# Kernel tuning notes

Hardware: AMD Instinct MI355X
Metric: run time of the kernel (lower is better)

Reference implementation:

```python
import jax, jax.numpy as jnp
import numpy as np

C = 32       # dim_features
D1 = 1024    # line grid resolution (dim1)
D2 = 256     # lowres plane resolution (dim2)
M = 64       # hidden width m
H = 1024
W = 1024
RESX = 1024.0
RESY = 1024.0


def setup_inputs() -> dict:
    key = jax.random.key(0)
    ks = jax.random.split(key, 8)
    coords = jax.random.uniform(ks[0], (H, W, 2), dtype=jnp.float32) * RESX
    # operation == 'multiply' init: rand*0.15 + 0.1
    line_feature_x = jax.random.uniform(ks[1], (C, D1), dtype=jnp.float32) * 0.15 + 0.1
    line_feature_y = jax.random.uniform(ks[2], (C, D1), dtype=jnp.float32) * 0.15 + 0.1
    plane_feature = jax.random.normal(ks[3], (C, D2, D2), dtype=jnp.float32) * 0.01
    W1 = jax.random.normal(ks[4], (M, C), dtype=jnp.float32) * (1.0 / np.sqrt(C))
    b1 = jnp.zeros((M,), dtype=jnp.float32)
    W2 = jax.random.normal(ks[5], (1, M), dtype=jnp.float32) * (1.0 / np.sqrt(M))
    b2 = jnp.zeros((1,), dtype=jnp.float32)
    return {"coords": coords, "line_feature_x": line_feature_x,
            "line_feature_y": line_feature_y, "plane_feature": plane_feature,
            "W1": W1, "b1": b1, "W2": W2, "b2": b2}


def _interp_line(table, gnorm):
    # table: [C, L]; gnorm: [H, W] in [-1, 1].
    # grid_sample(mode=bilinear, padding_mode=border, align_corners=True) on a
    # [1, C, L, 1] input reduces to 1D linear interp along L with clamped coords.
    L = table.shape[1]
    pos = jnp.clip((gnorm + 1.0) * 0.5 * (L - 1), 0.0, float(L - 1))
    i0 = jnp.minimum(jnp.floor(pos).astype(jnp.int32), L - 2)
    w = pos - i0.astype(pos.dtype)           # [H, W]
    return table[:, i0] * (1.0 - w) + table[:, i0 + 1] * w  # [C, H, W]


def _interp_plane(plane, xn, yn):
    # plane: [C, D, D]; xn/yn: [H, W] in [-1, 1].
    # grid_sample(mode=bilinear, padding_mode=zeros, align_corners=True).
    D = plane.shape[-1]
    px = (xn + 1.0) * 0.5 * (D - 1)
    py = (yn + 1.0) * 0.5 * (D - 1)
    x0 = jnp.floor(px).astype(jnp.int32)
    y0 = jnp.floor(py).astype(jnp.int32)
    wx = px - x0.astype(px.dtype)
    wy = py - y0.astype(py.dtype)

    def gather(yi, xi):
        valid = (xi >= 0) & (xi < D) & (yi >= 0) & (yi < D)   # zeros padding
        xc = jnp.clip(xi, 0, D - 1)
        yc = jnp.clip(yi, 0, D - 1)
        return plane[:, yc, xc] * valid                       # [C, H, W]

    return (gather(y0, x0) * (1.0 - wy) * (1.0 - wx)
            + gather(y0, x0 + 1) * (1.0 - wy) * wx
            + gather(y0 + 1, x0) * wy * (1.0 - wx)
            + gather(y0 + 1, x0 + 1) * wy * wx)


def reference(coords, line_feature_x, line_feature_y, plane_feature, W1, b1, W2, b2):
    xn = coords[..., 0] * 2.0 / RESX - 1.0   # [H, W]
    yn = coords[..., 1] * 2.0 / RESY - 1.0
    fx = _interp_line(line_feature_x, xn)    # [C, H, W]
    fy = _interp_line(line_feature_y, yn)    # [C, H, W]
    fp = _interp_plane(plane_feature, xn, yn)  # [C, H, W]
    # operation == 'multiply', mode == 'lowres'
    feat = (fx * fy + fp).transpose(1, 2, 0)  # [H, W, C]
    # nonconvex decoder: Linear(C->M) + ReLU + Linear(M->1)
    h = jax.nn.relu(jnp.einsum('hwc,mc->hwm', feat, W1) + b1)
    out = jnp.einsum('hwm,om->hwo', h, W2) + b2
    return out[..., 0]                        # [H, W]
```

## Files before the change

kernel.cpp:

```cpp
#include <hip/hip_runtime.h>

#define NC   32
#define ND1  1024
#define ND2  256
#define NM   64
#define NPIX (1024 * 1024)
#define NBUCK 256
#define CAP  4608
#define NSLOT (NBUCK * CAP)
#define PW   18
#define PPAD 33
#define FBLK 3
#define FTH  512

__device__ __forceinline__ int clampi(int v, int lo, int hi) {
    return min(max(v, lo), hi);
}

__global__ __launch_bounds__(256) void pass1_prepare(
    const float* __restrict__ plane, const float* __restrict__ lfx,
    const float* __restrict__ lfy, float* __restrict__ pl_t,
    float* __restrict__ lx_t, float* __restrict__ ly_t, int* __restrict__ cursor)
{
    __shared__ float tile[32][65];
    const int blk = blockIdx.x, tid = threadIdx.x;
    const float* in; float* out; int N, pos0;
    if (blk < 1024)      { in = plane; out = pl_t; N = 65536; pos0 = blk * 64; }
    else if (blk < 1040) { in = lfx;   out = lx_t; N = 1024;  pos0 = (blk - 1024) * 64; }
    else if (blk < 1056) { in = lfy;   out = ly_t; N = 1024;  pos0 = (blk - 1040) * 64; }
    else { if (tid < NBUCK) cursor[tid] = tid * CAP; return; }
#pragma unroll
    for (int r = 0; r < 8; ++r) {
        int c = r * 4 + (tid >> 6), p = tid & 63;
        tile[c][p] = in[c * N + pos0 + p];
    }
    __syncthreads();
#pragma unroll
    for (int r = 0; r < 8; ++r) {
        int p = r * 8 + (tid >> 5), c = tid & 31;
        out[(pos0 + p) * 32 + c] = tile[c][p];
    }
}

__global__ __launch_bounds__(1024) void scatter_slack(
    const float2* __restrict__ coords, int* __restrict__ cursor,
    float4* __restrict__ slots)
{
    __shared__ int h[NBUCK];
    __shared__ int basew[NBUCK];
    const int t = threadIdx.x;
    if (t < NBUCK) h[t] = 0;
    __syncthreads();
    const int base_i = blockIdx.x * 4096;
    float2 xy[4]; int cell[4];
#pragma unroll
    for (int r = 0; r < 4; ++r) {
        xy[r] = coords[base_i + r * 1024 + t];
        const int xi = clampi((int)xy[r].x, 0, 1023);
        const int yi = clampi((int)xy[r].y, 0, 1023);
        cell[r] = ((yi >> 6) << 4) | (xi >> 6);
        atomicAdd(&h[cell[r]], 1);
    }
    __syncthreads();
    if (t < NBUCK) {
        const int n = h[t];
        basew[t] = n ? atomicAdd(&cursor[t], n) : 0;
    }
    __syncthreads();
    if (t < NBUCK) h[t] = 0;
    __syncthreads();
#pragma unroll
    for (int r = 0; r < 4; ++r) {
        const int c   = cell[r];
        const int off = atomicAdd(&h[c], 1);
        const int dst = min(basew[c] + off, NSLOT - 1);
        slots[dst] = make_float4(xy[r].x, xy[r].y,
                                 __int_as_float(base_i + r * 1024 + t), 0.0f);
    }
}

__global__ __launch_bounds__(FTH) void fused_bucket(
    const float4* __restrict__ slots, const int* __restrict__ cursor,
    const float* __restrict__ lx,
    const float* __restrict__ ly,
    const float* __restrict__ pl,
    const float* __restrict__ W1, const float* __restrict__ b1,
    const float* __restrict__ W2, const float* __restrict__ b2,
    float* __restrict__ out)
{
    const int b    = blockIdx.x / FBLK;
    const int part = blockIdx.x - b * FBLK;
    const int t    = threadIdx.x;
    const int bx = b & 15, by = b >> 4;
    const int px0 = (int)(bx * 15.9375f);
    const int py0 = (int)(by * 15.9375f);

    __shared__ float pls[PW * PW * PPAD];
    for (int i = t; i < PW * PW * 8; i += FTH) {
        const int tex = i >> 3, k = i & 7;
        const int ty = tex / PW, tx = tex - ty * PW;
        const int gy = min(py0 + ty, ND2 - 1), gx = min(px0 + tx, ND2 - 1);
        const float4 v = ((const float4*)pl)[((gy << 8) + gx) * 8 + k];
        float* d = &pls[tex * PPAD + k * 4];
        d[0] = v.x; d[1] = v.y; d[2] = v.z; d[3] = v.w;
    }
    __syncthreads();

    const int base  = b * CAP;
    const int count = min(cursor[b] - base, CAP);
    const int s_end = (part + 1) * (CAP / FBLK);
    for (int s = part * (CAP / FBLK) + t; s < s_end; s += FTH) {
        if (s >= count) break;
        const float4 rec = slots[base + s];
        const float x = rec.x, y = rec.y;
        const int pix = __float_as_int(rec.z);

        const float xn = x * (2.0f / 1024.0f) - 1.0f;
        const float yn = y * (2.0f / 1024.0f) - 1.0f;

        float posx = fminf(fmaxf((xn + 1.0f) * 0.5f * 1023.0f, 0.0f), 1023.0f);
        int   ix   = min((int)posx, 1022);
        float wx   = posx - (float)ix;
        float omwx = 1.0f - wx;
        float posy = fminf(fmaxf((yn + 1.0f) * 0.5f * 1023.0f, 0.0f), 1023.0f);
        int   iy   = min((int)posy, 1022);
        float wy   = posy - (float)iy;
        float omwy = 1.0f - wy;

        float px  = (xn + 1.0f) * 0.5f * 255.0f;
        float py  = (yn + 1.0f) * 0.5f * 255.0f;
        float fx0 = floorf(px), fy0 = floorf(py);
        int   x0 = (int)fx0, y0 = (int)fy0;
        float pwx = px - fx0, pwy = py - fy0;
        int   x1 = x0 + 1, y1 = y0 + 1;
        float vx0 = (x0 >= 0 && x0 < ND2) ? 1.0f : 0.0f;
        float vx1 = (x1 >= 0 && x1 < ND2) ? 1.0f : 0.0f;
        float vy0 = (y0 >= 0 && y0 < ND2) ? 1.0f : 0.0f;
        float vy1 = (y1 >= 0 && y1 < ND2) ? 1.0f : 0.0f;
        int xc0 = clampi(x0, 0, ND2 - 1), xc1 = clampi(x1, 0, ND2 - 1);
        int yc0 = clampi(y0, 0, ND2 - 1), yc1 = clampi(y1, 0, ND2 - 1);
        float w00 = (1.0f - pwy) * (1.0f - pwx) * vy0 * vx0;
        float w01 = (1.0f - pwy) * pwx          * vy0 * vx1;
        float w10 = pwy          * (1.0f - pwx) * vy1 * vx0;
        float w11 = pwy          * pwx          * vy1 * vx1;

        const int tx0i = xc0 - px0, tx1i = xc1 - px0;
        const int ty0i = yc0 - py0, ty1i = yc1 - py0;
        const float* t00 = &pls[(ty0i * PW + tx0i) * PPAD];
        const float* t01 = &pls[(ty0i * PW + tx1i) * PPAD];
        const float* t10 = &pls[(ty1i * PW + tx0i) * PPAD];
        const float* t11 = &pls[(ty1i * PW + tx1i) * PPAD];

        const float4* ax0 = (const float4*)(lx + ix * NC);
        const float4* ax1 = (const float4*)(lx + (ix + 1) * NC);
        const float4* ay0 = (const float4*)(ly + iy * NC);
        const float4* ay1 = (const float4*)(ly + (iy + 1) * NC);

        float feat[NC];
#pragma unroll
        for (int k = 0; k < 8; ++k) {
            const float4 a0 = ax0[k], a1 = ax1[k];
            const float4 c0 = ay0[k], c1 = ay1[k];
            const int cb = k * 4;
#define FC(j, comp)                                                          \
            {                                                                \
                float fxv = a0.comp * omwx + a1.comp * wx;                   \
                float fyv = c0.comp * omwy + c1.comp * wy;                   \
                float fpv = t00[cb + j] * w00 + t01[cb + j] * w01 +          \
                            t10[cb + j] * w10 + t11[cb + j] * w11;           \
                feat[cb + j] = fxv * fyv + fpv;                              \
            }
            FC(0, x) FC(1, y) FC(2, z) FC(3, w)
#undef FC
        }

        float acc = b2[0];
#pragma unroll 4
        for (int m = 0; m < NM; ++m) {
            const float4* wrow = (const float4*)(W1 + m * NC);
            float a = b1[m];
#pragma unroll
            for (int k = 0; k < 8; ++k) {
                const float4 wv = wrow[k];
                a = fmaf(feat[k * 4 + 0], wv.x, a);
                a = fmaf(feat[k * 4 + 1], wv.y, a);
                a = fmaf(feat[k * 4 + 2], wv.z, a);
                a = fmaf(feat[k * 4 + 3], wv.w, a);
            }
            acc = fmaf(fmaxf(a, 0.0f), W2[m], acc);
        }
        out[pix] = acc;
    }
}

template <int MODE>
__global__ __launch_bounds__(256) void fused_forward(
    const float* __restrict__ coords, const float* __restrict__ lx,
    const float* __restrict__ ly, const float* __restrict__ pl,
    const float* __restrict__ W1, const float* __restrict__ b1,
    const float* __restrict__ W2, const float* __restrict__ b2,
    float* __restrict__ out)
{
    const int i = blockIdx.x * 256 + threadIdx.x;
    const float2 xy = reinterpret_cast<const float2*>(coords)[i];
    const float xn = xy.x * (2.0f / 1024.0f) - 1.0f;
    const float yn = xy.y * (2.0f / 1024.0f) - 1.0f;

    float posx = fminf(fmaxf((xn + 1.0f) * 0.5f * 1023.0f, 0.0f), 1023.0f);
    int   ix   = min((int)posx, 1022);
    float wx   = posx - (float)ix, omwx = 1.0f - wx;
    float posy = fminf(fmaxf((yn + 1.0f) * 0.5f * 1023.0f, 0.0f), 1023.0f);
    int   iy   = min((int)posy, 1022);
    float wy   = posy - (float)iy, omwy = 1.0f - wy;

    float px  = (xn + 1.0f) * 0.5f * 255.0f;
    float py  = (yn + 1.0f) * 0.5f * 255.0f;
    float fx0 = floorf(px), fy0 = floorf(py);
    int   x0 = (int)fx0, y0 = (int)fy0;
    float pwx = px - fx0, pwy = py - fy0;
    int   x1 = x0 + 1, y1 = y0 + 1;
    float vx0 = (x0 >= 0 && x0 < ND2) ? 1.0f : 0.0f;
    float vx1 = (x1 >= 0 && x1 < ND2) ? 1.0f : 0.0f;
    float vy0 = (y0 >= 0 && y0 < ND2) ? 1.0f : 0.0f;
    float vy1 = (y1 >= 0 && y1 < ND2) ? 1.0f : 0.0f;
    int xc0 = clampi(x0, 0, ND2 - 1), xc1 = clampi(x1, 0, ND2 - 1);
    int yc0 = clampi(y0, 0, ND2 - 1), yc1 = clampi(y1, 0, ND2 - 1);
    float w00 = (1.0f - pwy) * (1.0f - pwx) * vy0 * vx0;
    float w01 = (1.0f - pwy) * pwx          * vy0 * vx1;
    float w10 = pwy          * (1.0f - pwx) * vy1 * vx0;
    float w11 = pwy          * pwx          * vy1 * vx1;

    float feat[NC];
    if (MODE == 1) {
        const float4* ax0 = (const float4*)(lx + ix * NC);
        const float4* ax1 = (const float4*)(lx + (ix + 1) * NC);
        const float4* ay0 = (const float4*)(ly + iy * NC);
        const float4* ay1 = (const float4*)(ly + (iy + 1) * NC);
        const float4* p00 = (const float4*)(pl + (yc0 * ND2 + xc0) * NC);
        const float4* p01 = (const float4*)(pl + (yc0 * ND2 + xc1) * NC);
        const float4* p10 = (const float4*)(pl + (yc1 * ND2 + xc0) * NC);
        const float4* p11 = (const float4*)(pl + (yc1 * ND2 + xc1) * NC);
#pragma unroll
        for (int k = 0; k < 8; ++k) {
            float4 a0 = ax0[k], a1 = ax1[k], c0 = ay0[k], c1 = ay1[k];
            float4 q00 = p00[k], q01 = p01[k], q10 = p10[k], q11 = p11[k];
#define FC(j, comp)                                                          \
            {                                                                \
                float fxv = a0.comp * omwx + a1.comp * wx;                   \
                float fyv = c0.comp * omwy + c1.comp * wy;                   \
                float fpv = q00.comp * w00 + q01.comp * w01 +                \
                            q10.comp * w10 + q11.comp * w11;                 \
                feat[k * 4 + j] = fxv * fyv + fpv;                           \
            }
            FC(0, x) FC(1, y) FC(2, z) FC(3, w)
#undef FC
        }
    } else {
#pragma unroll
        for (int c = 0; c < NC; ++c) {
            float a0 = lx[c * ND1 + ix], a1 = lx[c * ND1 + ix + 1];
            float c0 = ly[c * ND1 + iy], c1 = ly[c * ND1 + iy + 1];
            const float* ps = pl + c * (ND2 * ND2);
            float q00 = ps[yc0 * ND2 + xc0], q01 = ps[yc0 * ND2 + xc1];
            float q10 = ps[yc1 * ND2 + xc0], q11 = ps[yc1 * ND2 + xc1];
            feat[c] = (a0 * omwx + a1 * wx) * (c0 * omwy + c1 * wy)
                    + (q00 * w00 + q01 * w01 + q10 * w10 + q11 * w11);
        }
    }

    float acc = b2[0];
#pragma unroll 4
    for (int m = 0; m < NM; ++m) {
        const float4* wrow = (const float4*)(W1 + m * NC);
        float a = b1[m];
#pragma unroll
        for (int k = 0; k < 8; ++k) {
            float4 wv = wrow[k];
            a = fmaf(feat[k * 4 + 0], wv.x, a);
            a = fmaf(feat[k * 4 + 1], wv.y, a);
            a = fmaf(feat[k * 4 + 2], wv.z, a);
            a = fmaf(feat[k * 4 + 3], wv.w, a);
        }
        acc = fmaf(fmaxf(a, 0.0f), W2[m], acc);
    }
    out[i] = acc;
}

extern "C" void kernel_launch(void* const* d_in, const int* in_sizes, int n_in,
                              void* d_out, int out_size, void* d_ws, size_t ws_size,
                              hipStream_t stream) {
    const float* coords = (const float*)d_in[0];
    const float* lfx    = (const float*)d_in[1];
    const float* lfy    = (const float*)d_in[2];
    const float* plane  = (const float*)d_in[3];
    const float* W1     = (const float*)d_in[4];
    const float* b1     = (const float*)d_in[5];
    const float* W2     = (const float*)d_in[6];
    const float* b2     = (const float*)d_in[7];
    float* out = (float*)d_out;

    const size_t planeBytes = (size_t)ND2 * ND2 * NC * sizeof(float);
    const size_t lineBytes  = (size_t)ND1 * NC * sizeof(float);
    const size_t slotsBytes = (size_t)NSLOT * sizeof(float4);
    const size_t needTrans  = planeBytes + 2 * lineBytes;
    const size_t needFull   = needTrans + slotsBytes + NBUCK * sizeof(int);

    if (ws_size >= needFull) {
        char* p = (char*)d_ws;
        float*  pl_t   = (float*)p;   p += planeBytes;
        float*  lx_t   = (float*)p;   p += lineBytes;
        float*  ly_t   = (float*)p;   p += lineBytes;
        float4* slots  = (float4*)p;  p += slotsBytes;
        int*    cursor = (int*)p;

        pass1_prepare<<<1057, 256, 0, stream>>>(plane, lfx, lfy,
                                                pl_t, lx_t, ly_t, cursor);
        scatter_slack<<<NPIX / 4096, 1024, 0, stream>>>((const float2*)coords,
                                                        cursor, slots);
        fused_bucket<<<NBUCK * FBLK, FTH, 0, stream>>>(slots, cursor, lx_t, ly_t,
                                                       pl_t, W1, b1, W2, b2, out);
    } else if (ws_size >= needTrans) {
        float* pl_t = (float*)d_ws;
        float* lx_t = (float*)((char*)d_ws + planeBytes);
        float* ly_t = lx_t + ND1 * NC;
        pass1_prepare<<<1056, 256, 0, stream>>>(plane, lfx, lfy,
                                                pl_t, lx_t, ly_t, nullptr);
        fused_forward<1><<<NPIX / 256, 256, 0, stream>>>(
            coords, lx_t, ly_t, pl_t, W1, b1, W2, b2, out);
    } else {
        fused_forward<0><<<NPIX / 256, 256, 0, stream>>>(
            coords, lfx, lfy, plane, W1, b1, W2, b2, out);
    }
}
```

Measured before the change: 187.0 us.

## Compute decoder MLP with split-bf16 MFMA and load plane tile directly

Replaces the per-thread scalar 32x64 MLP in the bucketed kernel with wave-level MFMA 16x16x32 bf16 ops. Each wave handles 16 pixels, lanes split the channel dimension, and a hi/lo bf16 split (three MFMAs) approximates fp32 accuracy. The second layer is reduced with lane shuffles. The plane tile is now read straight from the original channel-major plane into shared memory, so the full plane transpose in the prepare pass is skipped and that pass shrinks to the line tables plus the cursor init. In exchange there is extra pack/shuffle work and slightly reduced precision, and the plane loads into shared memory become strided.

```diff
diff --git a/kernel.cpp b/kernel.cpp
--- a/kernel.cpp
+++ b/kernel.cpp
@@ -9,12 +9,32 @@
 #define CAP  4608
 #define NSLOT (NBUCK * CAP)
 #define PW   18
-#define PPAD 33
+#define PPADF 36
 #define FBLK 3
 #define FTH  512
+#define PART_SLOTS (CAP / FBLK)
+#define PART_CHUNKS (PART_SLOTS/16)
+
+typedef __attribute__((ext_vector_type(8))) short bf16x8;
+typedef __attribute__((ext_vector_type(4))) float f32x4;
 
 __device__ __forceinline__ int clampi(int v, int lo, int hi) {
     return min(max(v, lo), hi);
+}
+
+__device__ __forceinline__ void pack_hilo(const float* f, bf16x8& hi, bf16x8& lo) {
+    union { unsigned int u[4]; bf16x8 v; } H, L;
+#pragma unroll
+    for (int j = 0; j < 4; ++j) {
+        unsigned int b0 = __float_as_uint(f[2 * j]);
+        unsigned int b1 = __float_as_uint(f[2 * j + 1]);
+        unsigned int h0 = b0 & 0xFFFF0000u, h1 = b1 & 0xFFFF0000u;
+        H.u[j] = (h0 >> 16) | h1;
+        float l0 = f[2 * j]     - __uint_as_float(h0);
+        float l1 = f[2 * j + 1] - __uint_as_float(h1);
+        L.u[j] = (__float_as_uint(l0) >> 16) | (__float_as_uint(l1) & 0xFFFF0000u);
+    }
+    hi = H.v; lo = L.v;
 }
 
 __global__ __launch_bounds__(256) void pass1_prepare(
@@ -25,10 +45,10 @@
     __shared__ float tile[32][65];
     const int blk = blockIdx.x, tid = threadIdx.x;
     const float* in; float* out; int N, pos0;
-    if (blk < 1024)      { in = plane; out = pl_t; N = 65536; pos0 = blk * 64; }
-    else if (blk < 1040) { in = lfx;   out = lx_t; N = 1024;  pos0 = (blk - 1024) * 64; }
-    else if (blk < 1056) { in = lfy;   out = ly_t; N = 1024;  pos0 = (blk - 1040) * 64; }
-    else { if (tid < NBUCK) cursor[tid] = tid * CAP; return; }
+    if (blk < 16)       { in = lfx;   out = lx_t; N = 1024;  pos0 = blk * 64; }
+    else if (blk < 32)  { in = lfy;   out = ly_t; N = 1024;  pos0 = (blk - 16) * 64; }
+    else if (blk == 32) { if (cursor && tid < NBUCK) cursor[tid] = tid * CAP; return; }
+    else                { in = plane; out = pl_t; N = 65536; pos0 = (blk - 33) * 64; }
 #pragma unroll
     for (int r = 0; r < 8; ++r) {
         int c = r * 4 + (tid >> 6), p = tid & 63;
@@ -79,11 +99,11 @@
     }
 }
 
-__global__ __launch_bounds__(FTH) void fused_bucket(
+__global__ __launch_bounds__(FTH, 4) void fused_mfma(
     const float4* __restrict__ slots, const int* __restrict__ cursor,
     const float* __restrict__ lx,
     const float* __restrict__ ly,
-    const float* __restrict__ pl,
+    const float* __restrict__ plane,
     const float* __restrict__ W1, const float* __restrict__ b1,
     const float* __restrict__ W2, const float* __restrict__ b2,
     float* __restrict__ out)
@@ -91,41 +111,56 @@
     const int b    = blockIdx.x / FBLK;
     const int part = blockIdx.x - b * FBLK;
     const int t    = threadIdx.x;
+    const int wid  = t >> 6;
+    const int lane = t & 63;
+    const int lcol = lane & 15;
+    const int lq   = lane >> 4;
     const int bx = b & 15, by = b >> 4;
     const int px0 = (int)(bx * 15.9375f);
     const int py0 = (int)(by * 15.9375f);
 
-    __shared__ float pls[PW * PW * PPAD];
-    for (int i = t; i < PW * PW * 8; i += FTH) {
-        const int tex = i >> 3, k = i & 7;
+    __shared__ float pls[PW * PW * PPADF];
+    for (int i = t; i < PW * PW * 32; i += FTH) {
+        const int c = i / (PW * PW), tex = i - c * (PW * PW);
         const int ty = tex / PW, tx = tex - ty * PW;
         const int gy = min(py0 + ty, ND2 - 1), gx = min(px0 + tx, ND2 - 1);
-        const float4 v = ((const float4*)pl)[((gy << 8) + gx) * 8 + k];
-        float* d = &pls[tex * PPAD + k * 4];
-        d[0] = v.x; d[1] = v.y; d[2] = v.z; d[3] = v.w;
-    }
+        pls[tex * PPADF + c] = plane[c * 65536 + (gy << 8) + gx];
+    }
+
+    bf16x8 bhi[4], blo[4];
+    float b1v[4], w2v[4];
+#pragma unroll
+    for (int nt = 0; nt < 4; ++nt) {
+        const int row = nt * 16 + lcol;
+        const float4* wr = (const float4*)(W1 + row * NC + lq * 8);
+        const float4 wa = wr[0], wb = wr[1];
+        float wf[8] = {wa.x, wa.y, wa.z, wa.w, wb.x, wb.y, wb.z, wb.w};
+        pack_hilo(wf, bhi[nt], blo[nt]);
+        b1v[nt] = b1[row];
+        w2v[nt] = W2[row];
+    }
+    const float b2s = b2[0];
     __syncthreads();
 
     const int base  = b * CAP;
     const int count = min(cursor[b] - base, CAP);
-    const int s_end = (part + 1) * (CAP / FBLK);
-    for (int s = part * (CAP / FBLK) + t; s < s_end; s += FTH) {
-        if (s >= count) break;
-        const float4 rec = slots[base + s];
+
+    for (int ci = wid; ci < PART_CHUNKS; ci += FTH / 64) {
+        const int chunk = part * PART_SLOTS + ci * 16;
+        if (chunk >= count) break;
+        const int s = chunk + lcol;
+        const float4 rec = slots[base + min(s, count - 1)];
         const float x = rec.x, y = rec.y;
-        const int pix = __float_as_int(rec.z);
 
         const float xn = x * (2.0f / 1024.0f) - 1.0f;
         const float yn = y * (2.0f / 1024.0f) - 1.0f;
 
         float posx = fminf(fmaxf((xn + 1.0f) * 0.5f * 1023.0f, 0.0f), 1023.0f);
         int   ix   = min((int)posx, 1022);
-        float wx   = posx - (float)ix;
-        float omwx = 1.0f - wx;
+        float wx   = posx - (float)ix, omwx = 1.0f - wx;
         float posy = fminf(fmaxf((yn + 1.0f) * 0.5f * 1023.0f, 0.0f), 1023.0f);
         int   iy   = min((int)posy, 1022);
-        float wy   = posy - (float)iy;
-        float omwy = 1.0f - wy;
+        float wy   = posy - (float)iy, omwy = 1.0f - wy;
 
         float px  = (xn + 1.0f) * 0.5f * 255.0f;
         float py  = (yn + 1.0f) * 0.5f * 255.0f;
@@ -144,52 +179,65 @@
         float w10 = pwy          * (1.0f - pwx) * vy1 * vx0;
         float w11 = pwy          * pwx          * vy1 * vx1;
 
-        const int tx0i = xc0 - px0, tx1i = xc1 - px0;
-        const int ty0i = yc0 - py0, ty1i = yc1 - py0;
-        const float* t00 = &pls[(ty0i * PW + tx0i) * PPAD];
-        const float* t01 = &pls[(ty0i * PW + tx1i) * PPAD];
-        const float* t10 = &pls[(ty1i * PW + tx0i) * PPAD];
-        const float* t11 = &pls[(ty1i * PW + tx1i) * PPAD];
-
-        const float4* ax0 = (const float4*)(lx + ix * NC);
-        const float4* ax1 = (const float4*)(lx + (ix + 1) * NC);
-        const float4* ay0 = (const float4*)(ly + iy * NC);
-        const float4* ay1 = (const float4*)(ly + (iy + 1) * NC);
-
-        float feat[NC];
-#pragma unroll
-        for (int k = 0; k < 8; ++k) {
-            const float4 a0 = ax0[k], a1 = ax1[k];
-            const float4 c0 = ay0[k], c1 = ay1[k];
-            const int cb = k * 4;
-#define FC(j, comp)                                                          \
-            {                                                                \
-                float fxv = a0.comp * omwx + a1.comp * wx;                   \
-                float fyv = c0.comp * omwy + c1.comp * wy;                   \
-                float fpv = t00[cb + j] * w00 + t01[cb + j] * w01 +          \
-                            t10[cb + j] * w10 + t11[cb + j] * w11;           \
-                feat[cb + j] = fxv * fyv + fpv;                              \
-            }
-            FC(0, x) FC(1, y) FC(2, z) FC(3, w)
-#undef FC
-        }
-
-        float acc = b2[0];
-#pragma unroll 4
-        for (int m = 0; m < NM; ++m) {
-            const float4* wrow = (const float4*)(W1 + m * NC);
-            float a = b1[m];
-#pragma unroll
-            for (int k = 0; k < 8; ++k) {
-                const float4 wv = wrow[k];
-                a = fmaf(feat[k * 4 + 0], wv.x, a);
-                a = fmaf(feat[k * 4 + 1], wv.y, a);
-                a = fmaf(feat[k * 4 + 2], wv.z, a);
-                a = fmaf(feat[k * 4 + 3], wv.w, a);
-            }
-            acc = fmaf(fmaxf(a, 0.0f), W2[m], acc);
-        }
-        out[pix] = acc;
+        const int ko = lq * 8;
+        const float4* LX0 = (const float4*)(lx + ix * NC + ko);
+        const float4* LX1 = (const float4*)(lx + (ix + 1) * NC + ko);
+        const float4* LY0 = (const float4*)(ly + iy * NC + ko);
+        const float4* LY1 = (const float4*)(ly + (iy + 1) * NC + ko);
+        const float4 xa = LX0[0], xb = LX0[1], Xa = LX1[0], Xb = LX1[1];
+        const float4 ya = LY0[0], yb = LY0[1], Ya = LY1[0], Yb = LY1[1];
+
+        const int t00o = ((yc0 - py0) * PW + (xc0 - px0)) * PPADF + ko;
+        const int t01o = ((yc0 - py0) * PW + (xc1 - px0)) * PPADF + ko;
+        const int t10o = ((yc1 - py0) * PW + (xc0 - px0)) * PPADF + ko;
+        const int t11o = ((yc1 - py0) * PW + (xc1 - px0)) * PPADF + ko;
+        const float4 q00a = *(const float4*)&pls[t00o], q00b = *(const float4*)&pls[t00o + 4];
+        const float4 q01a = *(const float4*)&pls[t01o], q01b = *(const float4*)&pls[t01o + 4];
+        const float4 q10a = *(const float4*)&pls[t10o], q10b = *(const float4*)&pls[t10o + 4];
+        const float4 q11a = *(const float4*)&pls[t11o], q11b = *(const float4*)&pls[t11o + 4];
+
+        const float a0[8] = {xa.x, xa.y, xa.z, xa.w, xb.x, xb.y, xb.z, xb.w};
+        const float a1[8] = {Xa.x, Xa.y, Xa.z, Xa.w, Xb.x, Xb.y, Xb.z, Xb.w};
+        const float c0[8] = {ya.x, ya.y, ya.z, ya.w, yb.x, yb.y, yb.z, yb.w};
+        const float c1[8] = {Ya.x, Ya.y, Ya.z, Ya.w, Yb.x, Yb.y, Yb.z, Yb.w};
+        const float p00[8] = {q00a.x, q00a.y, q00a.z, q00a.w, q00b.x, q00b.y, q00b.z, q00b.w};
+        const float p01[8] = {q01a.x, q01a.y, q01a.z, q01a.w, q01b.x, q01b.y, q01b.z, q01b.w};
+        const float p10[8] = {q10a.x, q10a.y, q10a.z, q10a.w, q10b.x, q10b.y, q10b.z, q10b.w};
+        const float p11[8] = {q11a.x, q11a.y, q11a.z, q11a.w, q11b.x, q11b.y, q11b.z, q11b.w};
+
+        float f[8];
+#pragma unroll
+        for (int j = 0; j < 8; ++j) {
+            const float fxv = a0[j] * omwx + a1[j] * wx;
+            const float fyv = c0[j] * omwy + c1[j] * wy;
+            const float fpv = p00[j] * w00 + p01[j] * w01 + p10[j] * w10 + p11[j] * w11;
+            f[j] = fxv * fyv + fpv;
+        }
+
+        bf16x8 ahi, alo;
+        pack_hilo(f, ahi, alo);
+
+        float psum[4] = {0.0f, 0.0f, 0.0f, 0.0f};
+#pragma unroll
+        for (int nt = 0; nt < 4; ++nt) {
+            f32x4 acc = {b1v[nt], b1v[nt], b1v[nt], b1v[nt]};
+            acc = __builtin_amdgcn_mfma_f32_16x16x32_bf16(ahi, bhi[nt], acc, 0, 0, 0);
+            acc = __builtin_amdgcn_mfma_f32_16x16x32_bf16(ahi, blo[nt], acc, 0, 0, 0);
+            acc = __builtin_amdgcn_mfma_f32_16x16x32_bf16(alo, bhi[nt], acc, 0, 0, 0);
+#pragma unroll
+            for (int r = 0; r < 4; ++r)
+                psum[r] = fmaf(fmaxf(acc[r], 0.0f), w2v[nt], psum[r]);
+        }
+
+#pragma unroll
+        for (int m = 1; m <= 8; m <<= 1) {
+#pragma unroll
+            for (int r = 0; r < 4; ++r)
+                psum[r] += __shfl_xor(psum[r], m, 64);
+        }
+
+        if (lq == (lcol >> 2) && s < count)
+            out[__float_as_int(rec.z)] = psum[lcol & 3] + b2s;
     }
 }
 
@@ -313,17 +361,17 @@
         float4* slots  = (float4*)p;  p += slotsBytes;
         int*    cursor = (int*)p;
 
-        pass1_prepare<<<1057, 256, 0, stream>>>(plane, lfx, lfy,
-                                                pl_t, lx_t, ly_t, cursor);
+        pass1_prepare<<<33, 256, 0, stream>>>(plane, lfx, lfy,
+                                              pl_t, lx_t, ly_t, cursor);
         scatter_slack<<<NPIX / 4096, 1024, 0, stream>>>((const float2*)coords,
                                                         cursor, slots);
-        fused_bucket<<<NBUCK * FBLK, FTH, 0, stream>>>(slots, cursor, lx_t, ly_t,
-                                                       pl_t, W1, b1, W2, b2, out);
+        fused_mfma<<<NBUCK * FBLK, FTH, 0, stream>>>(slots, cursor, lx_t, ly_t,
+                                                     plane, W1, b1, W2, b2, out);
     } else if (ws_size >= needTrans) {
         float* pl_t = (float*)d_ws;
         float* lx_t = (float*)((char*)d_ws + planeBytes);
         float* ly_t = lx_t + ND1 * NC;
-        pass1_prepare<<<1056, 256, 0, stream>>>(plane, lfx, lfy,
+        pass1_prepare<<<1057, 256, 0, stream>>>(plane, lfx, lfy,
                                                 pl_t, lx_t, ly_t, nullptr);
         fused_forward<1><<<NPIX / 256, 256, 0, stream>>>(
             coords, lx_t, ly_t, pl_t, W1, b1, W2, b2, out);
```

New measurement: 195.1 us. 4.3% more time.
